# Kernel optimization log

Measured on AMD Instinct MI355X. Metric: run time of the kernel, lower is better.

## Reference

```python
import jax, jax.numpy as jnp
import numpy as np

SW, FB, EMB, H = 96, 64, 512, 3   # seg_width, freq_bandwidth, embedding_dim, num_heads
B, T = 4, 1024
F = SW * FB


def setup_inputs() -> dict:
    key = jax.random.key(0)
    ks = jax.random.split(key, 12)
    s = 0.02
    dh = SW // H
    return {
        "x": jax.random.normal(ks[0], (B, T, F), jnp.float32),
        "o_enc": jax.random.randint(ks[1], (B, T), 0, 2, jnp.int32),
        "r_enc": jax.random.normal(ks[2], (B, T, EMB), jnp.float32),
        "Wq": jax.random.normal(ks[3], (SW, SW), jnp.float32) * s,
        "bq": jnp.zeros((SW,), jnp.float32),
        "Wk": jax.random.normal(ks[4], (SW, SW), jnp.float32) * s,
        "bk": jnp.zeros((SW,), jnp.float32),
        "Wv": jax.random.normal(ks[5], (SW, SW), jnp.float32) * s,
        "bv": jnp.zeros((SW,), jnp.float32),
        "Er": jax.random.normal(ks[6], (FB, dh), jnp.float32) * s,   # relative pos embeddings, max_len = FB
        "W1": jax.random.normal(ks[7], (SW, 4 * SW), jnp.float32) * s,
        "b1": jnp.zeros((4 * SW,), jnp.float32),
        "W2": jax.random.normal(ks[8], (4 * SW, SW), jnp.float32) * s,
        "b2": jnp.zeros((SW,), jnp.float32),
        "We": jax.random.normal(ks[9], (F, EMB), jnp.float32) * s,
        "be": jnp.zeros((EMB,), jnp.float32),
    }


def _skew(qer):
    # qer: (N, h, L, L) -> Srel via Music-Transformer skewing
    padded = jnp.pad(qer, ((0, 0), (0, 0), (0, 0), (1, 0)))      # (N,h,L,L+1)
    n, h, l, l1 = padded.shape
    return padded.reshape(n, h, l1, l)[:, :, 1:, :]               # (N,h,L,L)


def _rel_attention(x, Wq, bq, Wk, bk, Wv, bv, Er):
    # x: (N, L, D); relative global self-attention with causal mask
    N, L, D = x.shape
    dh = D // H

    def heads(t):
        return t.reshape(N, L, H, dh).transpose(0, 2, 1, 3)       # (N,h,L,dh)

    q = heads(x @ Wq + bq)
    k = heads(x @ Wk + bk)
    v = heads(x @ Wv + bv)
    qer = jnp.einsum('nhld,md->nhlm', q, Er)                      # (N,h,L,L)
    srel = _skew(qer)
    scores = (jnp.einsum('nhld,nhmd->nhlm', q, k) + srel) / jnp.sqrt(jnp.asarray(dh, x.dtype))
    causal = jnp.triu(jnp.ones((L, L), bool), 1)
    scores = jnp.where(causal, jnp.finfo(scores.dtype).min, scores)
    attn = jax.nn.softmax(scores, axis=-1)
    out = jnp.einsum('nhlm,nhmd->nhld', attn, v)
    return out.transpose(0, 2, 1, 3).reshape(N, L, D)


def _segmentwise_mean(data, block_ids):
    # data: (B,T,E), block_ids: (B,T) contiguous non-decreasing segment ids in [0,T)
    Bn, Tn, En = data.shape
    seg_sum = jax.vmap(lambda d, i: jax.ops.segment_sum(d, i, num_segments=Tn))(data, block_ids)
    cnt = jax.vmap(lambda i: jax.ops.segment_sum(jnp.ones_like(i), i, num_segments=Tn))(block_ids)
    means = seg_sum / jnp.maximum(cnt, 1).astype(data.dtype)[..., None]
    is_start = jnp.concatenate(
        [jnp.ones((Bn, 1), bool), block_ids[:, 1:] != block_ids[:, :-1]], axis=1)
    gathered = jnp.take_along_axis(means, block_ids[..., None], axis=1)   # (B,T,E)
    # original writes each block's mean only at the block's first position, zeros elsewhere
    return jnp.where(is_start[..., None], gathered, jnp.zeros((), data.dtype))


def reference(x, o_enc, r_enc, Wq, bq, Wk, bk, Wv, bv, Er, W1, b1, W2, b2, We, be):
    Bn, Tn, Fn = x.shape
    xr = x.reshape(Bn * Tn, SW, FB).transpose(0, 2, 1)            # (B*T, FB, SW)
    emb = _rel_attention(xr, Wq, bq, Wk, bk, Wv, bv, Er)
    emb = jax.nn.relu(emb @ W1 + b1) @ W2 + b2                    # FFN: SW -> 4SW -> SW
    emb = emb.transpose(0, 2, 1).reshape(Bn, Tn, Fn)
    emb = emb @ We + be                                           # (B,T,EMB)
    # nn.LayerNorm(emb.shape): normalize over the WHOLE tensor, no affine, eps=1e-8
    mu = emb.mean()
    var = ((emb - mu) ** 2).mean()
    emb = (emb - mu) / jnp.sqrt(var + 1e-8)
    # _regionalize: block ids from cumsum of binary boundary indicators
    block_ids = jnp.cumsum(o_enc, axis=1)
    block_ids = block_ids - block_ids[:, :1]                      # matches 'if b[0]==1: b -= 1'
    block_means = _segmentwise_mean(emb, block_ids)
    return block_means + r_enc + emb
```

## Files before the change

kernel.cpp:

```cpp
#include <hip/hip_runtime.h>
#include <hip/hip_bf16.h>


typedef __attribute__((ext_vector_type(8))) short bf16x8;
typedef __attribute__((ext_vector_type(4))) float f32x4;

struct PtrTab { const void* p[16]; };

enum : int {
  O_WQT = 0,
  O_BQ  = 9984,
  O_WKT = 10080,
  O_BK  = 20064,
  O_WVT = 20160,
  O_BV  = 30144,
  O_ER  = 30240,
  O_W1T = 32288,
  O_B1  = 72224,
  O_W2C = 72608,
  O_B2  = 118688,
  O_WET = 118784
};

__device__ __forceinline__ float b2f(__hip_bfloat16 v) { return __bfloat162float(v); }
__device__ __forceinline__ __hip_bfloat16 f2b(float v) { return __float2bfloat16(v); }

__device__ __forceinline__ void gload16(const void* g, void* l) {
    __builtin_amdgcn_global_load_lds(
        (const __attribute__((address_space(1))) void*)g,
        (__attribute__((address_space(3))) void*)l, 16, 0, 0);
}

__global__ __launch_bounds__(256) void prep_kernel(PtrTab tab,
                                                   __hip_bfloat16* __restrict__ Wc,
                                                   float* __restrict__ sums,
                                                   int* __restrict__ bids)
{
    __shared__ __hip_bfloat16 tile[64][65];
    const int bid = blockIdx.x, tid = threadIdx.x;
    const int kt = bid % 96, nt = bid / 96;
    const float* We = (const float*)tab.p[14];
    const int k0 = kt * 64, n0 = nt * 64;
    for (int e = tid; e < 4096; e += 256) {
        int kk = e >> 6, nn = e & 63;
        tile[nn][kk] = f2b(We[(size_t)(k0 + kk) * 512 + n0 + nn]);
    }
    __syncthreads();
    __hip_bfloat16* dstT = Wc + O_WET + ((size_t)nt * 96 + kt) * 4096;
    for (int e = tid; e < 4096; e += 256) dstT[e] = tile[e >> 6][e & 63];

    const int g = bid * 256 + tid;
    const int stride = gridDim.x * 256;
    const float* Wq = (const float*)tab.p[3];
    const float* bq = (const float*)tab.p[4];
    const float* Wk = (const float*)tab.p[5];
    const float* bk = (const float*)tab.p[6];
    const float* Wv = (const float*)tab.p[7];
    const float* bv = (const float*)tab.p[8];
    const float* Er = (const float*)tab.p[9];
    const float* W1 = (const float*)tab.p[10];
    const float* b1 = (const float*)tab.p[11];
    const float* W2 = (const float*)tab.p[12];
    const float* b2 = (const float*)tab.p[13];

    for (int t = 0; t < 3; ++t) {
        const float* W = (t == 0 ? Wq : t == 1 ? Wk : Wv);
        __hip_bfloat16* d = Wc + t * 10080;
        for (int i = g; i < 9984; i += stride) {
            int j = i / 104, c = i - j * 104;
            d[i] = (c < 96) ? f2b(W[c * 96 + j]) : f2b(0.0f);
        }
    }
    for (int i = g; i < 96; i += stride) {
        Wc[O_BQ + i] = f2b(bq[i]);
        Wc[O_BK + i] = f2b(bk[i]);
        Wc[O_BV + i] = f2b(bv[i]);
        Wc[O_B2 + i] = f2b(b2[i]);
    }
    for (int i = g; i < 2048; i += stride) Wc[O_ER + i] = f2b(Er[i]);
    for (int i = g; i < 39936; i += stride) {
        int j = i / 104, c = i - j * 104;
        Wc[O_W1T + i] = (c < 96) ? f2b(W1[c * 384 + j]) : f2b(0.0f);
    }
    for (int i = g; i < 384; i += stride) Wc[O_B1 + i] = f2b(b1[i]);
    for (int i = g; i < 46080; i += stride) {
        int kc = i / 3840, r = i - kc * 3840;
        int nn = r / 40, kk = r - nn * 40;
        Wc[O_W2C + i] = (kk < 32) ? f2b(W2[(kc * 32 + kk) * 96 + nn]) : f2b(0.0f);
    }
    if (g < 2) sums[g] = 0.f;

    if (bid < 4) {
        __syncthreads();
        int* ts = (int*)tile;
        const int* o = (const int*)tab.p[1] + bid * 1024;
        int v0 = o[4 * tid], v1 = o[4 * tid + 1], v2 = o[4 * tid + 2], v3 = o[4 * tid + 3];
        int p0 = v0, p1 = p0 + v1, p2 = p1 + v2, p3 = p2 + v3;
        ts[tid] = p3;
        __syncthreads();
        for (int off = 1; off < 256; off <<= 1) {
            int mine = ts[tid];
            int add = (tid >= off) ? ts[tid - off] : 0;
            __syncthreads();
            ts[tid] = mine + add;
            __syncthreads();
        }
        const int excl = (tid > 0) ? ts[tid - 1] : 0;
        const int off0 = o[0];
        int* bd = bids + bid * 1024;
        bd[4 * tid]     = excl + p0 - off0;
        bd[4 * tid + 1] = excl + p1 - off0;
        bd[4 * tid + 2] = excl + p2 - off0;
        bd[4 * tid + 3] = excl + p3 - off0;
    }
}

__global__ __launch_bounds__(256, 4) void attn_ffn_kernel(
    const float* __restrict__ x, const __hip_bfloat16* __restrict__ Wc,
    __hip_bfloat16* __restrict__ M)
{
    const int n = blockIdx.x, tid = threadIdx.x;
    const int w = tid >> 6, lane = tid & 63, quad = lane >> 4, ln = lane & 15;

    __shared__ __align__(16) char smem[40448];
    __hip_bfloat16* xs  = (__hip_bfloat16*)(smem);
    __hip_bfloat16* wb  = (__hip_bfloat16*)(smem);
    __hip_bfloat16* kS  = (__hip_bfloat16*)(smem + 13312);
    __hip_bfloat16* vT  = (__hip_bfloat16*)(smem + 26624);
    __hip_bfloat16* hid = (__hip_bfloat16*)(smem + 13312);

    const f32x4 z4 = {0.f, 0.f, 0.f, 0.f};
    const int rowb = 16 * w + quad * 4;
    const int myrow = 16 * w + ln;

    bf16x8 wf[9], wfn[9];
    #pragma unroll
    for (int i = 0; i < 9; ++i)
        wf[i] = *(const bf16x8*)(Wc + O_WQT + ((i % 3) * 16 + ln) * 104 + (i / 3) * 32 + quad * 8);

    {
        const float* xb = x + (size_t)n * 6144;
        const int sb = w * 24;
        for (int c = 0; c < 3; ++c) {
            float v[8];
            #pragma unroll
            for (int j = 0; j < 8; ++j) v[j] = xb[(sb + c * 8 + j) * 64 + lane];
            union { __hip_bfloat16 h[8]; bf16x8 v8; } pk;
            #pragma unroll
            for (int j = 0; j < 8; ++j) pk.h[j] = f2b(v[j]);
            *(bf16x8*)(xs + lane * 104 + sb + c * 8) = pk.v8;
        }
    }
    __syncthreads();

    bf16x8 af[3];
    #pragma unroll
    for (int ks = 0; ks < 3; ++ks)
        af[ks] = *(const bf16x8*)(xs + myrow * 104 + ks * 32 + quad * 8);

    bf16x8 aqr[3];

    for (int st = 0; st < 6; ++st) {
        const int t = st >> 1, half = st & 1;
        if (st < 5) {
            const __hip_bfloat16* nb = Wc + ((st + 1) >> 1) * 10080 + ((st + 1) & 1) * 4992;
            #pragma unroll
            for (int i = 0; i < 9; ++i)
                wfn[i] = *(const bf16x8*)(nb + ((i % 3) * 16 + ln) * 104 + (i / 3) * 32 + quad * 8);
        }
        f32x4 acc[3] = {z4, z4, z4};
        const int j0 = half * 48;
        const __hip_bfloat16* bt = Wc + 9984 + t * 10080;
        if (t < 2) {
            #pragma unroll
            for (int ks = 0; ks < 3; ++ks)
                #pragma unroll
                for (int ct = 0; ct < 3; ++ct)
                    acc[ct] = __builtin_amdgcn_mfma_f32_16x16x32_bf16(wf[ks * 3 + ct], af[ks], acc[ct], 0, 0, 0);
            #pragma unroll
            for (int ct = 0; ct < 3; ++ct) {
                const int cb = j0 + ct * 16 + 4 * quad;
                union { uint2 u; __hip_bfloat16 h[4]; } bu;
                bu.u = *(const uint2*)(bt + cb);
                union { __hip_bfloat16 h4[4]; uint2 u; } pk;
                #pragma unroll
                for (int r = 0; r < 4; ++r) pk.h4[r] = f2b(acc[ct][r] + b2f(bu.h[r]));
                *(uint2*)(kS + myrow * 104 + cb) = pk.u;
            }
        } else {
            #pragma unroll
            for (int ks = 0; ks < 3; ++ks)
                #pragma unroll
                for (int ct = 0; ct < 3; ++ct)
                    acc[ct] = __builtin_amdgcn_mfma_f32_16x16x32_bf16(af[ks], wf[ks * 3 + ct], acc[ct], 0, 0, 0);
            #pragma unroll
            for (int ct = 0; ct < 3; ++ct) {
                int col = j0 + ct * 16 + ln;
                float bb = b2f(bt[col]);
                union { __hip_bfloat16 h4[4]; uint2 u; } pk;
                #pragma unroll
                for (int r = 0; r < 4; ++r) pk.h4[r] = f2b(acc[ct][r] + bb);
                *(uint2*)(vT + col * 72 + rowb) = pk.u;
            }
        }
        if (t == 0 && half == 1) {
            #pragma unroll
            for (int h = 0; h < 3; ++h)
                aqr[h] = *(const bf16x8*)(kS + myrow * 104 + h * 32 + quad * 8);
        }
        #pragma unroll
        for (int i = 0; i < 9; ++i) wf[i] = wfn[i];
    }

    bf16x8 erf[4];
    #pragma unroll
    for (int tn = 0; tn < 4; ++tn)
        erf[tn] = *(const bf16x8*)(Wc + O_ER + (16 * tn + ln) * 32 + quad * 8);
    __syncthreads();

    bf16x8 pf0, pf1, pf2;
    {
        const bf16x8* src = (const bf16x8*)(Wc + O_W1T);
        pf0 = src[tid]; pf1 = src[tid + 256];
        if (tid + 512 < 624) pf2 = src[tid + 512];
    }

    __hip_bfloat16* S2 = xs + 32;
    const int ql = myrow;
    const int sshift = 63 - ql;
    f32x4 oacc[3][2] = {{z4, z4}, {z4, z4}, {z4, z4}};

    #pragma unroll
    for (int h = 0; h < 3; ++h) {
        const int c0 = h * 32;
        bf16x8 aq = aqr[h];
        #pragma unroll
        for (int tn = 0; tn < 4; ++tn) {
            f32x4 q4 = __builtin_amdgcn_mfma_f32_16x16x32_bf16(erf[tn], aq, z4, 0, 0, 0);
            #pragma unroll
            for (int r = 0; r < 4; ++r) {
                int e = 16 * tn + 4 * quad + r;
                if (e >= sshift) S2[ql * 104 + (e - sshift)] = f2b(q4[r]);
            }
        }
        float sco[4][4];
        #pragma unroll
        for (int tn = 0; tn < 4; ++tn) {
            bf16x8 kf = *(const bf16x8*)(kS + (16 * tn + ln) * 104 + c0 + quad * 8);
            f32x4 s1 = __builtin_amdgcn_mfma_f32_16x16x32_bf16(kf, aq, z4, 0, 0, 0);
            #pragma unroll
            for (int r = 0; r < 4; ++r) sco[tn][r] = s1[r];
        }
        #pragma unroll
        for (int tn = 0; tn < 4; ++tn) {
            union { __hip_bfloat16 h4[4]; uint2 u; } sr;
            sr.u = *(const uint2*)(S2 + ql * 104 + 16 * tn + 4 * quad);
            #pragma unroll
            for (int r = 0; r < 4; ++r) {
                int m = 16 * tn + 4 * quad + r;
                sco[tn][r] = (m <= ql)
                    ? (sco[tn][r] + b2f(sr.h4[r])) * 0.17677669529663687f
                    : -3.0e38f;
            }
        }
        float mt[4];
        #pragma unroll
        for (int tn = 0; tn < 4; ++tn)
            mt[tn] = fmaxf(fmaxf(sco[tn][0], sco[tn][1]), fmaxf(sco[tn][2], sco[tn][3]));
        float mx = fmaxf(fmaxf(mt[0], mt[1]), fmaxf(mt[2], mt[3]));
        mx = fmaxf(mx, __shfl_xor(mx, 16, 64));
        mx = fmaxf(mx, __shfl_xor(mx, 32, 64));
        float st_[4];
        #pragma unroll
        for (int tn = 0; tn < 4; ++tn) {
            #pragma unroll
            for (int r = 0; r < 4; ++r) sco[tn][r] = __expf(sco[tn][r] - mx);
            st_[tn] = (sco[tn][0] + sco[tn][1]) + (sco[tn][2] + sco[tn][3]);
        }
        float sum = (st_[0] + st_[1]) + (st_[2] + st_[3]);
        sum += __shfl_xor(sum, 16, 64);
        sum += __shfl_xor(sum, 32, 64);
        const float inv = 1.0f / sum;
        #pragma unroll
        for (int tn = 0; tn < 4; ++tn) {
            union { __hip_bfloat16 h4[4]; uint2 u; } pk;
            #pragma unroll
            for (int r = 0; r < 4; ++r) pk.h4[r] = f2b(sco[tn][r] * inv);
            *(uint2*)(S2 + ql * 104 + 16 * tn + 4 * quad) = pk.u;
        }
        #pragma unroll
        for (int ks2 = 0; ks2 < 2; ++ks2) {
            bf16x8 pa = *(const bf16x8*)(S2 + ql * 104 + ks2 * 32 + quad * 8);
            #pragma unroll
            for (int t2 = 0; t2 < 2; ++t2) {
                bf16x8 vb = *(const bf16x8*)(vT + (c0 + 16 * t2 + ln) * 72 + ks2 * 32 + quad * 8);
                oacc[h][t2] = __builtin_amdgcn_mfma_f32_16x16x32_bf16(vb, pa, oacc[h][t2], 0, 0, 0);
            }
        }
    }
    #pragma unroll
    for (int h = 0; h < 3; ++h)
        #pragma unroll
        for (int t2 = 0; t2 < 2; ++t2) {
            union { __hip_bfloat16 h4[4]; uint2 u; } pk;
            #pragma unroll
            for (int r = 0; r < 4; ++r) pk.h4[r] = f2b(oacc[h][t2][r]);
            *(uint2*)(xs + myrow * 104 + h * 32 + 16 * t2 + 4 * quad) = pk.u;
        }

    bf16x8 cf[3];
    #pragma unroll
    for (int ks = 0; ks < 3; ++ks)
        cf[ks] = *(const bf16x8*)(xs + myrow * 104 + ks * 32 + quad * 8);

    f32x4 acc2[6] = {z4, z4, z4, z4, z4, z4};
    bf16x8 w2f[6], w2fn[6];
    for (int jh = 0; jh < 2; ++jh) {
        for (int cc = 0; cc < 4; ++cc) {
            const int j0g = jh * 192 + cc * 48;
            __syncthreads();
            {
                bf16x8* dst = (bf16x8*)wb;
                dst[tid] = pf0;
                dst[tid + 256] = pf1;
                if (tid + 512 < 624) dst[tid + 512] = pf2;
                if (cc < 3) {
                    const bf16x8* src = (const bf16x8*)(Wc + O_W1T + jh * 19968 + (cc + 1) * 4992);
                    pf0 = src[tid]; pf1 = src[tid + 256];
                    if (tid + 512 < 624) pf2 = src[tid + 512];
                } else {
                    const __hip_bfloat16* nb = Wc + O_W2C + (jh * 6) * 3840;
                    #pragma unroll
                    for (int ct = 0; ct < 6; ++ct)
                        w2f[ct] = *(const bf16x8*)(nb + (ct * 16 + ln) * 40 + quad * 8);
                }
            }
            __syncthreads();
            f32x4 a1[3] = {z4, z4, z4};
            #pragma unroll
            for (int ks = 0; ks < 3; ++ks) {
                #pragma unroll
                for (int ct = 0; ct < 3; ++ct) {
                    bf16x8 b = *(const bf16x8*)(wb + (ct * 16 + ln) * 104 + ks * 32 + quad * 8);
                    a1[ct] = __builtin_amdgcn_mfma_f32_16x16x32_bf16(b, cf[ks], a1[ct], 0, 0, 0);
                }
            }
            #pragma unroll
            for (int ct = 0; ct < 3; ++ct) {
                const int cb = ct * 16 + 4 * quad;
                union { uint2 u; __hip_bfloat16 h[4]; } bu;
                bu.u = *(const uint2*)(Wc + O_B1 + j0g + cb);
                union { __hip_bfloat16 h4[4]; uint2 u; } pk;
                #pragma unroll
                for (int r = 0; r < 4; ++r)
                    pk.h4[r] = f2b(fmaxf(a1[ct][r] + b2f(bu.h[r]), 0.f));
                *(uint2*)(hid + myrow * 200 + cc * 48 + cb) = pk.u;
            }
        }
        for (int kc = 0; kc < 6; ++kc) {
            if (kc < 5) {
                const __hip_bfloat16* nb = Wc + O_W2C + (jh * 6 + kc + 1) * 3840;
                #pragma unroll
                for (int ct = 0; ct < 6; ++ct)
                    w2fn[ct] = *(const bf16x8*)(nb + (ct * 16 + ln) * 40 + quad * 8);
            } else if (jh == 0) {
                const bf16x8* src = (const bf16x8*)(Wc + O_W1T + 19968);
                pf0 = src[tid]; pf1 = src[tid + 256];
                if (tid + 512 < 624) pf2 = src[tid + 512];
            }
            bf16x8 a = *(const bf16x8*)(hid + myrow * 200 + kc * 32 + quad * 8);
            #pragma unroll
            for (int ct = 0; ct < 6; ++ct)
                acc2[ct] = __builtin_amdgcn_mfma_f32_16x16x32_bf16(a, w2f[ct], acc2[ct], 0, 0, 0);
            if (kc < 5) {
                #pragma unroll
                for (int ct = 0; ct < 6; ++ct) w2f[ct] = w2fn[ct];
            }
        }
    }

    __hip_bfloat16* Mg = M + (size_t)n * 6144;
    #pragma unroll
    for (int ct = 0; ct < 6; ++ct) {
        int d = ct * 16 + ln;
        float bb = b2f(Wc[O_B2 + d]);
        union { __hip_bfloat16 h4[4]; uint2 u; } pk;
        #pragma unroll
        for (int r = 0; r < 4; ++r) pk.h4[r] = f2b(acc2[ct][r] + bb);
        *(uint2*)((char*)Mg + (size_t)(d * 64 + rowb) * 2) = pk.u;
    }
}

__global__ __launch_bounds__(256) void gemm_kernel(
    const __hip_bfloat16* __restrict__ A,
    const __hip_bfloat16* __restrict__ Wc,
    const float* __restrict__ be,
    float* __restrict__ Y,
    float* __restrict__ sums)
{
    __shared__ __align__(16) char gsm[65536];
    const int row0 = blockIdx.x * 64, nt = blockIdx.y, col0 = nt * 64;
    const int tid = threadIdx.x;
    const int w = tid >> 6, lane = tid & 63, quad = lane >> 4, ln = lane & 15;
    const __hip_bfloat16* Bsrc = Wc + O_WET + (size_t)nt * 96 * 4096;

    const f32x4 z4 = {0.f, 0.f, 0.f, 0.f};
    f32x4 acc[4] = {z4, z4, z4, z4};

    auto stage = [&](int buf, int kt) {
        char* Ab = gsm + buf * 16384;
        char* Bb = gsm + 32768 + buf * 16384;
        #pragma unroll
        for (int j = 0; j < 4; ++j) {
            const int b = j * 4096 + tid * 16;
            const int row = b >> 8;
            const int s = b ^ ((row & 7) << 4);
            const int col = (s & 255) >> 1;
            gload16(A + (size_t)(row0 + row) * 6144 + kt * 128 + col,
                    Ab + j * 4096 + w * 1024);
            gload16(Bsrc + (size_t)(2 * kt + (col >> 6)) * 4096 + row * 64 + (col & 63),
                    Bb + j * 4096 + w * 1024);
        }
    };

    stage(0, 0);
    __syncthreads();

    for (int kt = 0; kt < 48; ++kt) {
        const int cur = kt & 1;
        if (kt < 47) stage(cur ^ 1, kt + 1);
        const char* Ab = gsm + cur * 16384;
        const char* Bb = gsm + 32768 + cur * 16384;
        #pragma unroll
        for (int ks = 0; ks < 4; ++ks) {
            const int ra = ((16 * w + ln) << 8) + ks * 64 + quad * 16;
            bf16x8 a = *(const bf16x8*)(Ab + (ra ^ ((ln & 7) << 4)));
            #pragma unroll
            for (int tn = 0; tn < 4; ++tn) {
                const int rb = ((16 * tn + ln) << 8) + ks * 64 + quad * 16;
                bf16x8 b = *(const bf16x8*)(Bb + (rb ^ ((ln & 7) << 4)));
                acc[tn] = __builtin_amdgcn_mfma_f32_16x16x32_bf16(a, b, acc[tn], 0, 0, 0);
            }
        }
        __syncthreads();
    }

    float s = 0.f, s2 = 0.f;
    #pragma unroll
    for (int tn = 0; tn < 4; ++tn) {
        int col = col0 + 16 * tn + ln;
        float bb = be[col];
        #pragma unroll
        for (int r = 0; r < 4; ++r) {
            float v = acc[tn][r] + bb;
            Y[(size_t)(row0 + 16 * w + quad * 4 + r) * 512 + col] = v;
            s += v; s2 += v * v;
        }
    }
    #pragma unroll
    for (int off = 1; off < 64; off <<= 1) {
        s  += __shfl_xor(s, off, 64);
        s2 += __shfl_xor(s2, off, 64);
    }
    float* r1s = (float*)gsm;
    float* r2s = r1s + 4;
    if (lane == 0) { r1s[w] = s; r2s[w] = s2; }
    __syncthreads();
    if (tid == 0) {
        atomicAdd(&sums[0], r1s[0] + r1s[1] + r1s[2] + r1s[3]);
        atomicAdd(&sums[1], r2s[0] + r2s[1] + r2s[2] + r2s[3]);
    }
}

__global__ __launch_bounds__(256) void final_kernel(
    const float* __restrict__ Y, const int* __restrict__ bids,
    const float* __restrict__ sums, const float* __restrict__ r_enc,
    float* __restrict__ out)
{
    const int bt = blockIdx.x;
    const int b = bt >> 10, t = bt & 1023;
    const float mu = sums[0] * (1.0f / 2097152.0f);
    const float var = sums[1] * (1.0f / 2097152.0f) - mu * mu;
    const float rstd = rsqrtf(var + 1e-8f);
    const int* bid = bids + b * 1024;
    const int my = bid[t];
    const bool is_start = (t == 0) || (bid[t - 1] != my);
    int t2 = t + 1;
    float invc = 0.f;
    if (is_start) {
        while (t2 < 1024 && bid[t2] == my) ++t2;
        invc = 1.0f / (float)(t2 - t);
    }
    for (int e = threadIdx.x; e < 512; e += 256) {
        const size_t base = (size_t)bt * 512 + e;
        float res = (Y[base] - mu) * rstd + r_enc[base];
        if (is_start) {
            float s = 0.f;
            for (int tt = t; tt < t2; ++tt)
                s += (Y[((size_t)(b * 1024 + tt)) * 512 + e] - mu) * rstd;
            res += s * invc;
        }
        out[base] = res;
    }
}

extern "C" void kernel_launch(void* const* d_in, const int* in_sizes, int n_in,
                              void* d_out, int out_size, void* d_ws, size_t ws_size,
                              hipStream_t stream) {
    PtrTab tab;
    for (int i = 0; i < 16; ++i) tab.p[i] = d_in[i];

    char* ws = (char*)d_ws;
    __hip_bfloat16* M  = (__hip_bfloat16*)ws;
    float* Y           = (float*)(ws + 50331648);
    float* sums        = (float*)(ws + 58720256);
    int*   bids        = (int*)(ws + 58720320);
    __hip_bfloat16* Wc = (__hip_bfloat16*)(ws + 58736768);

    prep_kernel<<<768, 256, 0, stream>>>(tab, Wc, sums, bids);
    attn_ffn_kernel<<<4096, 256, 0, stream>>>((const float*)d_in[0], Wc, M);
    gemm_kernel<<<dim3(64, 8), 256, 0, stream>>>(M, Wc, (const float*)d_in[15], Y, sums);
    final_kernel<<<4096, 256, 0, stream>>>(Y, bids, sums, (const float*)d_in[2], (float*)d_out);
}
```

Baseline: 371.5 us.

## Split-K the embedding GEMM with separate reduce kernel; add MFMA priority hints

```diff
diff --git a/kernel.cpp b/kernel.cpp
--- a/kernel.cpp
+++ b/kernel.cpp
@@ -234,6 +234,7 @@
     for (int h = 0; h < 3; ++h) {
         const int c0 = h * 32;
         bf16x8 aq = aqr[h];
+        __builtin_amdgcn_s_setprio(1);
         #pragma unroll
         for (int tn = 0; tn < 4; ++tn) {
             f32x4 q4 = __builtin_amdgcn_mfma_f32_16x16x32_bf16(erf[tn], aq, z4, 0, 0, 0);
@@ -251,6 +252,7 @@
             #pragma unroll
             for (int r = 0; r < 4; ++r) sco[tn][r] = s1[r];
         }
+        __builtin_amdgcn_s_setprio(0);
         #pragma unroll
         for (int tn = 0; tn < 4; ++tn) {
             union { __hip_bfloat16 h4[4]; uint2 u; } sr;
@@ -288,6 +290,7 @@
             for (int r = 0; r < 4; ++r) pk.h4[r] = f2b(sco[tn][r] * inv);
             *(uint2*)(S2 + ql * 104 + 16 * tn + 4 * quad) = pk.u;
         }
+        __builtin_amdgcn_s_setprio(1);
         #pragma unroll
         for (int ks2 = 0; ks2 < 2; ++ks2) {
             bf16x8 pa = *(const bf16x8*)(S2 + ql * 104 + ks2 * 32 + quad * 8);
@@ -297,6 +300,7 @@
                 oacc[h][t2] = __builtin_amdgcn_mfma_f32_16x16x32_bf16(vb, pa, oacc[h][t2], 0, 0, 0);
             }
         }
+        __builtin_amdgcn_s_setprio(0);
     }
     #pragma unroll
     for (int h = 0; h < 3; ++h)
@@ -391,6 +395,98 @@
     }
 }
 
+__global__ __launch_bounds__(256) void gemm_split_kernel(
+    const __hip_bfloat16* __restrict__ A,
+    const __hip_bfloat16* __restrict__ Wc,
+    float* __restrict__ Yp)
+{
+    __shared__ __align__(16) char gsm[32768];
+    const int row0 = blockIdx.x * 64, nt = blockIdx.y, kh = blockIdx.z;
+    const int col0 = nt * 64;
+    const int tid = threadIdx.x;
+    const int w = tid >> 6, lane = tid & 63, quad = lane >> 4, ln = lane & 15;
+    const __hip_bfloat16* Bsrc = Wc + O_WET + (size_t)nt * 96 * 4096;
+    const int kt0 = kh * 48;
+    const size_t ka0 = (size_t)kh * 3072;
+
+    const f32x4 z4 = {0.f, 0.f, 0.f, 0.f};
+    f32x4 acc[4] = {z4, z4, z4, z4};
+
+    auto stage = [&](int buf, int kt) {
+        char* Ab = gsm + buf * 8192;
+        char* Bb = gsm + 16384 + buf * 8192;
+        #pragma unroll
+        for (int p = 0; p < 2; ++p) {
+            const int b = p * 4096 + tid * 16;
+            const int row = b >> 7;
+            const int cb = (b & 127) ^ ((row & 7) << 4);
+            const int col = cb >> 1;
+            gload16(A + (size_t)(row0 + row) * 6144 + ka0 + kt * 64 + col,
+                    Ab + p * 4096 + w * 1024);
+            gload16(Bsrc + (size_t)(kt0 + kt) * 4096 + row * 64 + col,
+                    Bb + p * 4096 + w * 1024);
+        }
+    };
+
+    stage(0, 0);
+    __syncthreads();
+
+    for (int kt = 0; kt < 48; ++kt) {
+        const int cur = kt & 1;
+        if (kt < 47) stage(cur ^ 1, kt + 1);
+        const char* Ab = gsm + cur * 8192;
+        const char* Bb = gsm + 16384 + cur * 8192;
+        #pragma unroll
+        for (int ks = 0; ks < 2; ++ks) {
+            const int ra = ((16 * w + ln) << 7) + ks * 64 + quad * 16;
+            bf16x8 a = *(const bf16x8*)(Ab + (ra ^ ((ln & 7) << 4)));
+            #pragma unroll
+            for (int tn = 0; tn < 4; ++tn) {
+                const int rb = ((16 * tn + ln) << 7) + ks * 64 + quad * 16;
+                bf16x8 b = *(const bf16x8*)(Bb + (rb ^ ((ln & 7) << 4)));
+                acc[tn] = __builtin_amdgcn_mfma_f32_16x16x32_bf16(a, b, acc[tn], 0, 0, 0);
+            }
+        }
+        __syncthreads();
+    }
+
+    float* Yh = Yp + (size_t)kh * 2097152;
+    #pragma unroll
+    for (int tn = 0; tn < 4; ++tn) {
+        int col = col0 + 16 * tn + ln;
+        #pragma unroll
+        for (int r = 0; r < 4; ++r)
+            Yh[(size_t)(row0 + 16 * w + quad * 4 + r) * 512 + col] = acc[tn][r];
+    }
+}
+
+__global__ __launch_bounds__(256) void sum_kernel(
+    const float* __restrict__ Yp, const float* __restrict__ be,
+    float* __restrict__ Y, float* __restrict__ sums)
+{
+    const int base = blockIdx.x * 1024;
+    float s = 0.f, s2 = 0.f;
+    #pragma unroll
+    for (int j = 0; j < 4; ++j) {
+        const int i = base + j * 256 + threadIdx.x;
+        float v = Yp[i] + Yp[i + 2097152] + be[i & 511];
+        Y[i] = v; s += v; s2 += v * v;
+    }
+    #pragma unroll
+    for (int off = 1; off < 64; off <<= 1) {
+        s  += __shfl_xor(s, off, 64);
+        s2 += __shfl_xor(s2, off, 64);
+    }
+    __shared__ float r1s[4], r2s[4];
+    const int w = threadIdx.x >> 6, lane = threadIdx.x & 63;
+    if (lane == 0) { r1s[w] = s; r2s[w] = s2; }
+    __syncthreads();
+    if (threadIdx.x == 0) {
+        atomicAdd(&sums[0], r1s[0] + r1s[1] + r1s[2] + r1s[3]);
+        atomicAdd(&sums[1], r2s[0] + r2s[1] + r2s[2] + r2s[3]);
+    }
+}
+
 __global__ __launch_bounds__(256) void gemm_kernel(
     const __hip_bfloat16* __restrict__ A,
     const __hip_bfloat16* __restrict__ Wc,
@@ -516,9 +612,15 @@
     float* sums        = (float*)(ws + 58720256);
     int*   bids        = (int*)(ws + 58720320);
     __hip_bfloat16* Wc = (__hip_bfloat16*)(ws + 58736768);
+    float* Yp          = (float*)(ws + 67108864);
 
     prep_kernel<<<768, 256, 0, stream>>>(tab, Wc, sums, bids);
     attn_ffn_kernel<<<4096, 256, 0, stream>>>((const float*)d_in[0], Wc, M);
-    gemm_kernel<<<dim3(64, 8), 256, 0, stream>>>(M, Wc, (const float*)d_in[15], Y, sums);
+    if (ws_size >= (size_t)84 * 1024 * 1024) {
+        gemm_split_kernel<<<dim3(64, 8, 2), 256, 0, stream>>>(M, Wc, Yp);
+        sum_kernel<<<2048, 256, 0, stream>>>(Yp, (const float*)d_in[15], Y, sums);
+    } else {
+        gemm_kernel<<<dim3(64, 8), 256, 0, stream>>>(M, Wc, (const float*)d_in[15], Y, sums);
+    }
     final_kernel<<<4096, 256, 0, stream>>>(Y, bids, sums, (const float*)d_in[2], (float*)d_out);
 }
```

Result: slower. 419.5 us (+12.9%).

## Retile embedding GEMM to 128x128 tiles with 8 waves and swizzled block order

Applied to the files above, without the earlier changes.

```diff
diff --git a/kernel.cpp b/kernel.cpp
--- a/kernel.cpp
+++ b/kernel.cpp
@@ -391,7 +391,7 @@
     }
 }
 
-__global__ __launch_bounds__(256) void gemm_kernel(
+__global__ __launch_bounds__(512) void gemm_kernel(
     const __hip_bfloat16* __restrict__ A,
     const __hip_bfloat16* __restrict__ Wc,
     const float* __restrict__ be,
@@ -399,76 +399,91 @@
     float* __restrict__ sums)
 {
     __shared__ __align__(16) char gsm[65536];
-    const int row0 = blockIdx.x * 64, nt = blockIdx.y, col0 = nt * 64;
+    __shared__ float r1s[8], r2s[8];
+    const int d = blockIdx.x;
+    const int c = d & 7, q = d >> 3;
+    const int by = q & 3;
+    const int rb = c + 8 * (q >> 2);
+    const int row0 = rb * 128, col0 = by * 128;
     const int tid = threadIdx.x;
     const int w = tid >> 6, lane = tid & 63, quad = lane >> 4, ln = lane & 15;
-    const __hip_bfloat16* Bsrc = Wc + O_WET + (size_t)nt * 96 * 4096;
+    const int wr = w >> 2, wc = w & 3;
 
     const f32x4 z4 = {0.f, 0.f, 0.f, 0.f};
-    f32x4 acc[4] = {z4, z4, z4, z4};
+    f32x4 acc[4][2] = {{z4, z4}, {z4, z4}, {z4, z4}, {z4, z4}};
 
     auto stage = [&](int buf, int kt) {
         char* Ab = gsm + buf * 16384;
         char* Bb = gsm + 32768 + buf * 16384;
         #pragma unroll
-        for (int j = 0; j < 4; ++j) {
-            const int b = j * 4096 + tid * 16;
-            const int row = b >> 8;
-            const int s = b ^ ((row & 7) << 4);
-            const int col = (s & 255) >> 1;
-            gload16(A + (size_t)(row0 + row) * 6144 + kt * 128 + col,
-                    Ab + j * 4096 + w * 1024);
-            gload16(Bsrc + (size_t)(2 * kt + (col >> 6)) * 4096 + row * 64 + (col & 63),
-                    Bb + j * 4096 + w * 1024);
+        for (int p = 0; p < 2; ++p) {
+            const int b = p * 8192 + tid * 16;
+            const int row = b >> 7;
+            const int cb = (b & 127) ^ ((row & 7) << 4);
+            const int col = cb >> 1;
+            gload16(A + (size_t)(row0 + row) * 6144 + kt * 64 + col,
+                    Ab + p * 8192 + w * 1024);
+            gload16(Wc + O_WET + ((size_t)(2 * by + (row >> 6)) * 96 + kt) * 4096
+                        + (row & 63) * 64 + col,
+                    Bb + p * 8192 + w * 1024);
         }
     };
 
     stage(0, 0);
     __syncthreads();
 
-    for (int kt = 0; kt < 48; ++kt) {
+    const int key = (ln & 7) << 4;
+    for (int kt = 0; kt < 96; ++kt) {
         const int cur = kt & 1;
-        if (kt < 47) stage(cur ^ 1, kt + 1);
+        if (kt < 95) stage(cur ^ 1, kt + 1);
         const char* Ab = gsm + cur * 16384;
         const char* Bb = gsm + 32768 + cur * 16384;
         #pragma unroll
-        for (int ks = 0; ks < 4; ++ks) {
-            const int ra = ((16 * w + ln) << 8) + ks * 64 + quad * 16;
-            bf16x8 a = *(const bf16x8*)(Ab + (ra ^ ((ln & 7) << 4)));
-            #pragma unroll
-            for (int tn = 0; tn < 4; ++tn) {
-                const int rb = ((16 * tn + ln) << 8) + ks * 64 + quad * 16;
-                bf16x8 b = *(const bf16x8*)(Bb + (rb ^ ((ln & 7) << 4)));
-                acc[tn] = __builtin_amdgcn_mfma_f32_16x16x32_bf16(a, b, acc[tn], 0, 0, 0);
-            }
+        for (int ks = 0; ks < 2; ++ks) {
+            const int ko = ks * 64 + quad * 16;
+            bf16x8 a[4], bf[2];
+            #pragma unroll
+            for (int i = 0; i < 4; ++i)
+                a[i] = *(const bf16x8*)(Ab + (64 * wr + 16 * i + ln) * 128 + (ko ^ key));
+            #pragma unroll
+            for (int j = 0; j < 2; ++j)
+                bf[j] = *(const bf16x8*)(Bb + (32 * wc + 16 * j + ln) * 128 + (ko ^ key));
+            #pragma unroll
+            for (int i = 0; i < 4; ++i)
+                #pragma unroll
+                for (int j = 0; j < 2; ++j)
+                    acc[i][j] = __builtin_amdgcn_mfma_f32_16x16x32_bf16(a[i], bf[j], acc[i][j], 0, 0, 0);
         }
         __syncthreads();
     }
 
     float s = 0.f, s2 = 0.f;
     #pragma unroll
-    for (int tn = 0; tn < 4; ++tn) {
-        int col = col0 + 16 * tn + ln;
-        float bb = be[col];
-        #pragma unroll
-        for (int r = 0; r < 4; ++r) {
-            float v = acc[tn][r] + bb;
-            Y[(size_t)(row0 + 16 * w + quad * 4 + r) * 512 + col] = v;
-            s += v; s2 += v * v;
-        }
-    }
+    for (int i = 0; i < 4; ++i)
+        #pragma unroll
+        for (int j = 0; j < 2; ++j) {
+            const int colg = col0 + 32 * wc + 16 * j + ln;
+            const float bb = be[colg];
+            #pragma unroll
+            for (int r = 0; r < 4; ++r) {
+                float v = acc[i][j][r] + bb;
+                Y[(size_t)(row0 + 64 * wr + 16 * i + quad * 4 + r) * 512 + colg] = v;
+                s += v; s2 += v * v;
+            }
+        }
     #pragma unroll
     for (int off = 1; off < 64; off <<= 1) {
         s  += __shfl_xor(s, off, 64);
         s2 += __shfl_xor(s2, off, 64);
     }
-    float* r1s = (float*)gsm;
-    float* r2s = r1s + 4;
     if (lane == 0) { r1s[w] = s; r2s[w] = s2; }
     __syncthreads();
     if (tid == 0) {
-        atomicAdd(&sums[0], r1s[0] + r1s[1] + r1s[2] + r1s[3]);
-        atomicAdd(&sums[1], r2s[0] + r2s[1] + r2s[2] + r2s[3]);
+        float t1 = 0.f, t2 = 0.f;
+        #pragma unroll
+        for (int i = 0; i < 8; ++i) { t1 += r1s[i]; t2 += r2s[i]; }
+        atomicAdd(&sums[0], t1);
+        atomicAdd(&sums[1], t2);
     }
 }
 
@@ -519,6 +534,6 @@
 
     prep_kernel<<<768, 256, 0, stream>>>(tab, Wc, sums, bids);
     attn_ffn_kernel<<<4096, 256, 0, stream>>>((const float*)d_in[0], Wc, M);
-    gemm_kernel<<<dim3(64, 8), 256, 0, stream>>>(M, Wc, (const float*)d_in[15], Y, sums);
+    gemm_kernel<<<128, 512, 0, stream>>>(M, Wc, (const float*)d_in[15], Y, sums);
     final_kernel<<<4096, 256, 0, stream>>>(Y, bids, sums, (const float*)d_in[2], (float*)d_out);
 }
```

New measurement: 407.8 us. +9.7%, slower.

## Process two sequences per block in attention-FFN kernel to reuse weight fragments

Applied to the files above, without the earlier changes.

```diff
diff --git a/kernel.cpp b/kernel.cpp
--- a/kernel.cpp
+++ b/kernel.cpp
@@ -115,19 +115,23 @@
     }
 }
 
-__global__ __launch_bounds__(256, 4) void attn_ffn_kernel(
+__global__ __launch_bounds__(256, 2) void attn_ffn_kernel(
     const float* __restrict__ x, const __hip_bfloat16* __restrict__ Wc,
     __hip_bfloat16* __restrict__ M)
 {
-    const int n = blockIdx.x, tid = threadIdx.x;
+    const int n0b = blockIdx.x, tid = threadIdx.x;
     const int w = tid >> 6, lane = tid & 63, quad = lane >> 4, ln = lane & 15;
 
-    __shared__ __align__(16) char smem[40448];
-    __hip_bfloat16* xs  = (__hip_bfloat16*)(smem);
-    __hip_bfloat16* wb  = (__hip_bfloat16*)(smem);
-    __hip_bfloat16* kS  = (__hip_bfloat16*)(smem + 13312);
-    __hip_bfloat16* vT  = (__hip_bfloat16*)(smem + 26624);
-    __hip_bfloat16* hid = (__hip_bfloat16*)(smem + 13312);
+    __shared__ __align__(16) char smem[80896];
+    __hip_bfloat16* xs[2]  = { (__hip_bfloat16*)(smem),
+                               (__hip_bfloat16*)(smem + 40448) };
+    __hip_bfloat16* kS[2]  = { (__hip_bfloat16*)(smem + 13312),
+                               (__hip_bfloat16*)(smem + 40448 + 13312) };
+    __hip_bfloat16* vT[2]  = { (__hip_bfloat16*)(smem + 26624),
+                               (__hip_bfloat16*)(smem + 40448 + 26624) };
+    __hip_bfloat16* wb     =   (__hip_bfloat16*)(smem);
+    __hip_bfloat16* hid[2] = { (__hip_bfloat16*)(smem + 13312),
+                               (__hip_bfloat16*)(smem + 40448 + 13312) };
 
     const f32x4 z4 = {0.f, 0.f, 0.f, 0.f};
     const int rowb = 16 * w + quad * 4;
@@ -138,8 +142,9 @@
     for (int i = 0; i < 9; ++i)
         wf[i] = *(const bf16x8*)(Wc + O_WQT + ((i % 3) * 16 + ln) * 104 + (i / 3) * 32 + quad * 8);
 
-    {
-        const float* xb = x + (size_t)n * 6144;
+    #pragma unroll
+    for (int ii = 0; ii < 2; ++ii) {
+        const float* xb = x + (size_t)(n0b + ii * 2048) * 6144;
         const int sb = w * 24;
         for (int c = 0; c < 3; ++c) {
             float v[8];
@@ -148,17 +153,19 @@
             union { __hip_bfloat16 h[8]; bf16x8 v8; } pk;
             #pragma unroll
             for (int j = 0; j < 8; ++j) pk.h[j] = f2b(v[j]);
-            *(bf16x8*)(xs + lane * 104 + sb + c * 8) = pk.v8;
+            *(bf16x8*)(xs[ii] + lane * 104 + sb + c * 8) = pk.v8;
         }
     }
     __syncthreads();
 
-    bf16x8 af[3];
-    #pragma unroll
-    for (int ks = 0; ks < 3; ++ks)
-        af[ks] = *(const bf16x8*)(xs + myrow * 104 + ks * 32 + quad * 8);
-
-    bf16x8 aqr[3];
+    bf16x8 af[2][3];
+    #pragma unroll
+    for (int ii = 0; ii < 2; ++ii)
+        #pragma unroll
+        for (int ks = 0; ks < 3; ++ks)
+            af[ii][ks] = *(const bf16x8*)(xs[ii] + myrow * 104 + ks * 32 + quad * 8);
+
+    bf16x8 aqr[2][3];
 
     for (int st = 0; st < 6; ++st) {
         const int t = st >> 1, half = st & 1;
@@ -168,45 +175,54 @@
             for (int i = 0; i < 9; ++i)
                 wfn[i] = *(const bf16x8*)(nb + ((i % 3) * 16 + ln) * 104 + (i / 3) * 32 + quad * 8);
         }
-        f32x4 acc[3] = {z4, z4, z4};
         const int j0 = half * 48;
         const __hip_bfloat16* bt = Wc + 9984 + t * 10080;
         if (t < 2) {
             #pragma unroll
-            for (int ks = 0; ks < 3; ++ks)
-                #pragma unroll
-                for (int ct = 0; ct < 3; ++ct)
-                    acc[ct] = __builtin_amdgcn_mfma_f32_16x16x32_bf16(wf[ks * 3 + ct], af[ks], acc[ct], 0, 0, 0);
-            #pragma unroll
-            for (int ct = 0; ct < 3; ++ct) {
-                const int cb = j0 + ct * 16 + 4 * quad;
-                union { uint2 u; __hip_bfloat16 h[4]; } bu;
-                bu.u = *(const uint2*)(bt + cb);
-                union { __hip_bfloat16 h4[4]; uint2 u; } pk;
-                #pragma unroll
-                for (int r = 0; r < 4; ++r) pk.h4[r] = f2b(acc[ct][r] + b2f(bu.h[r]));
-                *(uint2*)(kS + myrow * 104 + cb) = pk.u;
+            for (int ii = 0; ii < 2; ++ii) {
+                f32x4 acc[3] = {z4, z4, z4};
+                #pragma unroll
+                for (int ks = 0; ks < 3; ++ks)
+                    #pragma unroll
+                    for (int ct = 0; ct < 3; ++ct)
+                        acc[ct] = __builtin_amdgcn_mfma_f32_16x16x32_bf16(wf[ks * 3 + ct], af[ii][ks], acc[ct], 0, 0, 0);
+                #pragma unroll
+                for (int ct = 0; ct < 3; ++ct) {
+                    const int cb = j0 + ct * 16 + 4 * quad;
+                    union { uint2 u; __hip_bfloat16 h[4]; } bu;
+                    bu.u = *(const uint2*)(bt + cb);
+                    union { __hip_bfloat16 h4[4]; uint2 u; } pk;
+                    #pragma unroll
+                    for (int r = 0; r < 4; ++r) pk.h4[r] = f2b(acc[ct][r] + b2f(bu.h[r]));
+                    *(uint2*)(kS[ii] + myrow * 104 + cb) = pk.u;
+                }
             }
         } else {
             #pragma unroll
-            for (int ks = 0; ks < 3; ++ks)
-                #pragma unroll
-                for (int ct = 0; ct < 3; ++ct)
-                    acc[ct] = __builtin_amdgcn_mfma_f32_16x16x32_bf16(af[ks], wf[ks * 3 + ct], acc[ct], 0, 0, 0);
-            #pragma unroll
-            for (int ct = 0; ct < 3; ++ct) {
-                int col = j0 + ct * 16 + ln;
-                float bb = b2f(bt[col]);
-                union { __hip_bfloat16 h4[4]; uint2 u; } pk;
-                #pragma unroll
-                for (int r = 0; r < 4; ++r) pk.h4[r] = f2b(acc[ct][r] + bb);
-                *(uint2*)(vT + col * 72 + rowb) = pk.u;
+            for (int ii = 0; ii < 2; ++ii) {
+                f32x4 acc[3] = {z4, z4, z4};
+                #pragma unroll
+                for (int ks = 0; ks < 3; ++ks)
+                    #pragma unroll
+                    for (int ct = 0; ct < 3; ++ct)
+                        acc[ct] = __builtin_amdgcn_mfma_f32_16x16x32_bf16(af[ii][ks], wf[ks * 3 + ct], acc[ct], 0, 0, 0);
+                #pragma unroll
+                for (int ct = 0; ct < 3; ++ct) {
+                    int col = j0 + ct * 16 + ln;
+                    float bb = b2f(bt[col]);
+                    union { __hip_bfloat16 h4[4]; uint2 u; } pk;
+                    #pragma unroll
+                    for (int r = 0; r < 4; ++r) pk.h4[r] = f2b(acc[ct][r] + bb);
+                    *(uint2*)(vT[ii] + col * 72 + rowb) = pk.u;
+                }
             }
         }
         if (t == 0 && half == 1) {
             #pragma unroll
-            for (int h = 0; h < 3; ++h)
-                aqr[h] = *(const bf16x8*)(kS + myrow * 104 + h * 32 + quad * 8);
+            for (int ii = 0; ii < 2; ++ii)
+                #pragma unroll
+                for (int h = 0; h < 3; ++h)
+                    aqr[ii][h] = *(const bf16x8*)(kS[ii] + myrow * 104 + h * 32 + quad * 8);
         }
         #pragma unroll
         for (int i = 0; i < 9; ++i) wf[i] = wfn[i];
@@ -225,95 +241,112 @@
         if (tid + 512 < 624) pf2 = src[tid + 512];
     }
 
-    __hip_bfloat16* S2 = xs + 32;
     const int ql = myrow;
     const int sshift = 63 - ql;
-    f32x4 oacc[3][2] = {{z4, z4}, {z4, z4}, {z4, z4}};
+    f32x4 oacc[2][3][2];
+    #pragma unroll
+    for (int ii = 0; ii < 2; ++ii)
+        #pragma unroll
+        for (int h = 0; h < 3; ++h)
+            #pragma unroll
+            for (int t2 = 0; t2 < 2; ++t2) oacc[ii][h][t2] = z4;
 
     #pragma unroll
     for (int h = 0; h < 3; ++h) {
         const int c0 = h * 32;
-        bf16x8 aq = aqr[h];
-        #pragma unroll
-        for (int tn = 0; tn < 4; ++tn) {
-            f32x4 q4 = __builtin_amdgcn_mfma_f32_16x16x32_bf16(erf[tn], aq, z4, 0, 0, 0);
-            #pragma unroll
-            for (int r = 0; r < 4; ++r) {
-                int e = 16 * tn + 4 * quad + r;
-                if (e >= sshift) S2[ql * 104 + (e - sshift)] = f2b(q4[r]);
-            }
-        }
-        float sco[4][4];
-        #pragma unroll
-        for (int tn = 0; tn < 4; ++tn) {
-            bf16x8 kf = *(const bf16x8*)(kS + (16 * tn + ln) * 104 + c0 + quad * 8);
-            f32x4 s1 = __builtin_amdgcn_mfma_f32_16x16x32_bf16(kf, aq, z4, 0, 0, 0);
-            #pragma unroll
-            for (int r = 0; r < 4; ++r) sco[tn][r] = s1[r];
-        }
-        #pragma unroll
-        for (int tn = 0; tn < 4; ++tn) {
-            union { __hip_bfloat16 h4[4]; uint2 u; } sr;
-            sr.u = *(const uint2*)(S2 + ql * 104 + 16 * tn + 4 * quad);
-            #pragma unroll
-            for (int r = 0; r < 4; ++r) {
-                int m = 16 * tn + 4 * quad + r;
-                sco[tn][r] = (m <= ql)
-                    ? (sco[tn][r] + b2f(sr.h4[r])) * 0.17677669529663687f
-                    : -3.0e38f;
-            }
-        }
-        float mt[4];
-        #pragma unroll
-        for (int tn = 0; tn < 4; ++tn)
-            mt[tn] = fmaxf(fmaxf(sco[tn][0], sco[tn][1]), fmaxf(sco[tn][2], sco[tn][3]));
-        float mx = fmaxf(fmaxf(mt[0], mt[1]), fmaxf(mt[2], mt[3]));
-        mx = fmaxf(mx, __shfl_xor(mx, 16, 64));
-        mx = fmaxf(mx, __shfl_xor(mx, 32, 64));
-        float st_[4];
-        #pragma unroll
-        for (int tn = 0; tn < 4; ++tn) {
-            #pragma unroll
-            for (int r = 0; r < 4; ++r) sco[tn][r] = __expf(sco[tn][r] - mx);
-            st_[tn] = (sco[tn][0] + sco[tn][1]) + (sco[tn][2] + sco[tn][3]);
-        }
-        float sum = (st_[0] + st_[1]) + (st_[2] + st_[3]);
-        sum += __shfl_xor(sum, 16, 64);
-        sum += __shfl_xor(sum, 32, 64);
-        const float inv = 1.0f / sum;
-        #pragma unroll
-        for (int tn = 0; tn < 4; ++tn) {
-            union { __hip_bfloat16 h4[4]; uint2 u; } pk;
-            #pragma unroll
-            for (int r = 0; r < 4; ++r) pk.h4[r] = f2b(sco[tn][r] * inv);
-            *(uint2*)(S2 + ql * 104 + 16 * tn + 4 * quad) = pk.u;
-        }
-        #pragma unroll
-        for (int ks2 = 0; ks2 < 2; ++ks2) {
-            bf16x8 pa = *(const bf16x8*)(S2 + ql * 104 + ks2 * 32 + quad * 8);
+        #pragma unroll
+        for (int ii = 0; ii < 2; ++ii) {
+            __hip_bfloat16* S2 = xs[ii] + 32;
+            bf16x8 aq = aqr[ii][h];
+            #pragma unroll
+            for (int tn = 0; tn < 4; ++tn) {
+                f32x4 q4 = __builtin_amdgcn_mfma_f32_16x16x32_bf16(erf[tn], aq, z4, 0, 0, 0);
+                #pragma unroll
+                for (int r = 0; r < 4; ++r) {
+                    int e = 16 * tn + 4 * quad + r;
+                    if (e >= sshift) S2[ql * 104 + (e - sshift)] = f2b(q4[r]);
+                }
+            }
+            float sco[4][4];
+            #pragma unroll
+            for (int tn = 0; tn < 4; ++tn) {
+                bf16x8 kf = *(const bf16x8*)(kS[ii] + (16 * tn + ln) * 104 + c0 + quad * 8);
+                f32x4 s1 = __builtin_amdgcn_mfma_f32_16x16x32_bf16(kf, aq, z4, 0, 0, 0);
+                #pragma unroll
+                for (int r = 0; r < 4; ++r) sco[tn][r] = s1[r];
+            }
+            #pragma unroll
+            for (int tn = 0; tn < 4; ++tn) {
+                union { __hip_bfloat16 h4[4]; uint2 u; } sr;
+                sr.u = *(const uint2*)(S2 + ql * 104 + 16 * tn + 4 * quad);
+                #pragma unroll
+                for (int r = 0; r < 4; ++r) {
+                    int m = 16 * tn + 4 * quad + r;
+                    sco[tn][r] = (m <= ql)
+                        ? (sco[tn][r] + b2f(sr.h4[r])) * 0.17677669529663687f
+                        : -3.0e38f;
+                }
+            }
+            float mt[4];
+            #pragma unroll
+            for (int tn = 0; tn < 4; ++tn)
+                mt[tn] = fmaxf(fmaxf(sco[tn][0], sco[tn][1]), fmaxf(sco[tn][2], sco[tn][3]));
+            float mx = fmaxf(fmaxf(mt[0], mt[1]), fmaxf(mt[2], mt[3]));
+            mx = fmaxf(mx, __shfl_xor(mx, 16, 64));
+            mx = fmaxf(mx, __shfl_xor(mx, 32, 64));
+            float st_[4];
+            #pragma unroll
+            for (int tn = 0; tn < 4; ++tn) {
+                #pragma unroll
+                for (int r = 0; r < 4; ++r) sco[tn][r] = __expf(sco[tn][r] - mx);
+                st_[tn] = (sco[tn][0] + sco[tn][1]) + (sco[tn][2] + sco[tn][3]);
+            }
+            float sum = (st_[0] + st_[1]) + (st_[2] + st_[3]);
+            sum += __shfl_xor(sum, 16, 64);
+            sum += __shfl_xor(sum, 32, 64);
+            const float inv = 1.0f / sum;
+            #pragma unroll
+            for (int tn = 0; tn < 4; ++tn) {
+                union { __hip_bfloat16 h4[4]; uint2 u; } pk;
+                #pragma unroll
+                for (int r = 0; r < 4; ++r) pk.h4[r] = f2b(sco[tn][r] * inv);
+                *(uint2*)(S2 + ql * 104 + 16 * tn + 4 * quad) = pk.u;
+            }
+            #pragma unroll
+            for (int ks2 = 0; ks2 < 2; ++ks2) {
+                bf16x8 pa = *(const bf16x8*)(S2 + ql * 104 + ks2 * 32 + quad * 8);
+                #pragma unroll
+                for (int t2 = 0; t2 < 2; ++t2) {
+                    bf16x8 vb = *(const bf16x8*)(vT[ii] + (c0 + 16 * t2 + ln) * 72 + ks2 * 32 + quad * 8);
+                    oacc[ii][h][t2] = __builtin_amdgcn_mfma_f32_16x16x32_bf16(vb, pa, oacc[ii][h][t2], 0, 0, 0);
+                }
+            }
+        }
+    }
+    #pragma unroll
+    for (int ii = 0; ii < 2; ++ii)
+        #pragma unroll
+        for (int h = 0; h < 3; ++h)
             #pragma unroll
             for (int t2 = 0; t2 < 2; ++t2) {
-                bf16x8 vb = *(const bf16x8*)(vT + (c0 + 16 * t2 + ln) * 72 + ks2 * 32 + quad * 8);
-                oacc[h][t2] = __builtin_amdgcn_mfma_f32_16x16x32_bf16(vb, pa, oacc[h][t2], 0, 0, 0);
-            }
-        }
-    }
-    #pragma unroll
-    for (int h = 0; h < 3; ++h)
-        #pragma unroll
-        for (int t2 = 0; t2 < 2; ++t2) {
-            union { __hip_bfloat16 h4[4]; uint2 u; } pk;
-            #pragma unroll
-            for (int r = 0; r < 4; ++r) pk.h4[r] = f2b(oacc[h][t2][r]);
-            *(uint2*)(xs + myrow * 104 + h * 32 + 16 * t2 + 4 * quad) = pk.u;
-        }
-
-    bf16x8 cf[3];
-    #pragma unroll
-    for (int ks = 0; ks < 3; ++ks)
-        cf[ks] = *(const bf16x8*)(xs + myrow * 104 + ks * 32 + quad * 8);
-
-    f32x4 acc2[6] = {z4, z4, z4, z4, z4, z4};
+                union { __hip_bfloat16 h4[4]; uint2 u; } pk;
+                #pragma unroll
+                for (int r = 0; r < 4; ++r) pk.h4[r] = f2b(oacc[ii][h][t2][r]);
+                *(uint2*)(xs[ii] + myrow * 104 + h * 32 + 16 * t2 + 4 * quad) = pk.u;
+            }
+
+    bf16x8 cf[2][3];
+    #pragma unroll
+    for (int ii = 0; ii < 2; ++ii)
+        #pragma unroll
+        for (int ks = 0; ks < 3; ++ks)
+            cf[ii][ks] = *(const bf16x8*)(xs[ii] + myrow * 104 + ks * 32 + quad * 8);
+
+    f32x4 acc2[2][6];
+    #pragma unroll
+    for (int ii = 0; ii < 2; ++ii)
+        #pragma unroll
+        for (int ct = 0; ct < 6; ++ct) acc2[ii][ct] = z4;
     bf16x8 w2f[6], w2fn[6];
     for (int jh = 0; jh < 2; ++jh) {
         for (int cc = 0; cc < 4; ++cc) {
@@ -336,25 +369,28 @@
                 }
             }
             __syncthreads();
-            f32x4 a1[3] = {z4, z4, z4};
-            #pragma unroll
-            for (int ks = 0; ks < 3; ++ks) {
+            #pragma unroll
+            for (int ii = 0; ii < 2; ++ii) {
+                f32x4 a1[3] = {z4, z4, z4};
+                #pragma unroll
+                for (int ks = 0; ks < 3; ++ks) {
+                    #pragma unroll
+                    for (int ct = 0; ct < 3; ++ct) {
+                        bf16x8 b = *(const bf16x8*)(wb + (ct * 16 + ln) * 104 + ks * 32 + quad * 8);
+                        a1[ct] = __builtin_amdgcn_mfma_f32_16x16x32_bf16(b, cf[ii][ks], a1[ct], 0, 0, 0);
+                    }
+                }
                 #pragma unroll
                 for (int ct = 0; ct < 3; ++ct) {
-                    bf16x8 b = *(const bf16x8*)(wb + (ct * 16 + ln) * 104 + ks * 32 + quad * 8);
-                    a1[ct] = __builtin_amdgcn_mfma_f32_16x16x32_bf16(b, cf[ks], a1[ct], 0, 0, 0);
-                }
-            }
-            #pragma unroll
-            for (int ct = 0; ct < 3; ++ct) {
-                const int cb = ct * 16 + 4 * quad;
-                union { uint2 u; __hip_bfloat16 h[4]; } bu;
-                bu.u = *(const uint2*)(Wc + O_B1 + j0g + cb);
-                union { __hip_bfloat16 h4[4]; uint2 u; } pk;
-                #pragma unroll
-                for (int r = 0; r < 4; ++r)
-                    pk.h4[r] = f2b(fmaxf(a1[ct][r] + b2f(bu.h[r]), 0.f));
-                *(uint2*)(hid + myrow * 200 + cc * 48 + cb) = pk.u;
+                    const int cb = ct * 16 + 4 * quad;
+                    union { uint2 u; __hip_bfloat16 h[4]; } bu;
+                    bu.u = *(const uint2*)(Wc + O_B1 + j0g + cb);
+                    union { __hip_bfloat16 h4[4]; uint2 u; } pk;
+                    #pragma unroll
+                    for (int r = 0; r < 4; ++r)
+                        pk.h4[r] = f2b(fmaxf(a1[ct][r] + b2f(bu.h[r]), 0.f));
+                    *(uint2*)(hid[ii] + myrow * 200 + cc * 48 + cb) = pk.u;
+                }
             }
         }
         for (int kc = 0; kc < 6; ++kc) {
@@ -368,10 +404,13 @@
                 pf0 = src[tid]; pf1 = src[tid + 256];
                 if (tid + 512 < 624) pf2 = src[tid + 512];
             }
-            bf16x8 a = *(const bf16x8*)(hid + myrow * 200 + kc * 32 + quad * 8);
-            #pragma unroll
-            for (int ct = 0; ct < 6; ++ct)
-                acc2[ct] = __builtin_amdgcn_mfma_f32_16x16x32_bf16(a, w2f[ct], acc2[ct], 0, 0, 0);
+            #pragma unroll
+            for (int ii = 0; ii < 2; ++ii) {
+                bf16x8 a = *(const bf16x8*)(hid[ii] + myrow * 200 + kc * 32 + quad * 8);
+                #pragma unroll
+                for (int ct = 0; ct < 6; ++ct)
+                    acc2[ii][ct] = __builtin_amdgcn_mfma_f32_16x16x32_bf16(a, w2f[ct], acc2[ii][ct], 0, 0, 0);
+            }
             if (kc < 5) {
                 #pragma unroll
                 for (int ct = 0; ct < 6; ++ct) w2f[ct] = w2fn[ct];
@@ -379,15 +418,18 @@
         }
     }
 
-    __hip_bfloat16* Mg = M + (size_t)n * 6144;
-    #pragma unroll
-    for (int ct = 0; ct < 6; ++ct) {
-        int d = ct * 16 + ln;
-        float bb = b2f(Wc[O_B2 + d]);
-        union { __hip_bfloat16 h4[4]; uint2 u; } pk;
-        #pragma unroll
-        for (int r = 0; r < 4; ++r) pk.h4[r] = f2b(acc2[ct][r] + bb);
-        *(uint2*)((char*)Mg + (size_t)(d * 64 + rowb) * 2) = pk.u;
+    #pragma unroll
+    for (int ii = 0; ii < 2; ++ii) {
+        __hip_bfloat16* Mg = M + (size_t)(n0b + ii * 2048) * 6144;
+        #pragma unroll
+        for (int ct = 0; ct < 6; ++ct) {
+            int d = ct * 16 + ln;
+            float bb = b2f(Wc[O_B2 + d]);
+            union { __hip_bfloat16 h4[4]; uint2 u; } pk;
+            #pragma unroll
+            for (int r = 0; r < 4; ++r) pk.h4[r] = f2b(acc2[ii][ct][r] + bb);
+            *(uint2*)((char*)Mg + (size_t)(d * 64 + rowb) * 2) = pk.u;
+        }
     }
 }
 
@@ -518,7 +560,7 @@
     __hip_bfloat16* Wc = (__hip_bfloat16*)(ws + 58736768);
 
     prep_kernel<<<768, 256, 0, stream>>>(tab, Wc, sums, bids);
-    attn_ffn_kernel<<<4096, 256, 0, stream>>>((const float*)d_in[0], Wc, M);
+    attn_ffn_kernel<<<2048, 256, 0, stream>>>((const float*)d_in[0], Wc, M);
     gemm_kernel<<<dim3(64, 8), 256, 0, stream>>>(M, Wc, (const float*)d_in[15], Y, sums);
     final_kernel<<<4096, 256, 0, stream>>>(Y, bids, sums, (const float*)d_in[2], (float*)d_out);
 }
```

Result: faster. 352.9 us (-5.0%).
